# Kernel optimization log

Measured on AMD Instinct MI355X. Metric: run time of the kernel, lower is better.

## Reference

```python
import jax, jax.numpy as jnp
import numpy as np

N_NODES = 20000
N_INPUT = 64
K_MAX = 12
BITS = 64
N_OUT = 10
BATCH = 64
T = 128


def setup_inputs() -> dict:
    key = jax.random.key(0)
    ks = jax.random.split(key, 8)
    x = jax.random.randint(ks[0], (BATCH, T, BITS), 0, 2, dtype=jnp.int32)
    w_in = jax.random.randint(ks[1], (BITS, N_INPUT), 0, 2, dtype=jnp.int32)
    adj_list = jax.random.randint(ks[2], (N_NODES, K_MAX), 0, N_NODES, dtype=jnp.int32)
    adj_mask = jax.random.randint(ks[3], (N_NODES, K_MAX), 0, 2, dtype=jnp.int32)
    lut = jax.random.randint(ks[4], (N_NODES, 2 ** K_MAX), 0, 2, dtype=jnp.int32)
    init_states = jax.random.randint(ks[5], (1, N_NODES), 0, 2, dtype=jnp.int32)
    W_out = jax.random.normal(ks[6], (N_OUT, N_NODES - N_INPUT), dtype=jnp.float32) * 0.02
    b_out = jnp.zeros((N_OUT,), dtype=jnp.float32)
    return {"x": x, "w_in": w_in, "adj_list": adj_list, "adj_mask": adj_mask,
            "lut": lut, "init_states": init_states, "W_out": W_out, "b_out": b_out}


def reference(x, w_in, adj_list, adj_mask, lut, init_states, W_out, b_out):
    B, T_, bits = x.shape
    N, k = adj_list.shape
    I = w_in.shape[1]
    # powers_of_2, big-endian order as in make_minimal_powers_of_two (flip)
    powers = (2 ** jnp.arange(k - 1, -1, -1)).astype(jnp.int32)  # [k]
    no_neigh = ~(adj_mask.astype(bool).any(axis=1))              # [N] nodes w/o neighbours keep state
    node_ids = jnp.arange(N)
    states0 = jnp.broadcast_to(init_states, (B, N)).astype(jnp.int32)

    def step(states, x_t):
        # inject input: bipartite mapping of input bits onto first I nodes (OR-combine)
        u = ((x_t @ w_in) > 0).astype(jnp.int32)                 # [B, I]
        states = states.at[:, :I].set(u)
        # gather incoming neighbour states per node (irregular gather)
        neigh = jnp.take(states, adj_list, axis=1)               # [B, N, k]
        neigh = neigh * adj_mask[None, :, :]
        # bit-pack into LUT index
        idx = (neigh * powers[None, None, :]).sum(axis=-1)       # [B, N], < 2^k
        new = lut[node_ids[None, :], idx]                        # [B, N] LUT lookup
        new = jnp.where(no_neigh[None, :], states, new)
        return new, None

    states, _ = jax.lax.scan(step, states0, jnp.swapaxes(x, 0, 1))
    # readout on reservoir (non-input) nodes at final timestep
    feats = states[:, I:].astype(jnp.float32)                    # [B, N-I]
    out = jax.nn.sigmoid(feats @ W_out.T + b_out)                # [B, n_outputs]
    return out
```

## Files before the change

### kernel.cpp

```cpp
#include <hip/hip_runtime.h>
#include <cstdint>
#include <cstddef>


#define N_NODES   20000
#define N_INPUT   64
#define K_MAX     12
#define T_STEPS   128
#define N_BATCH   64
#define N_OUT     10
#define N_FEAT    (N_NODES - N_INPUT)
#define DUMMY_NODE 20000
#define ST_STRIDE 20008
#define R_DEPTH   (T_STEPS + 1)

#define NBLK 256
#define NTHR 1024
#define NPB  78
#define NPB_PAD 80
#define GO_CNT 8
#define AS     32

typedef unsigned long long u64;

#define A_LOAD(p)    __hip_atomic_load((p), __ATOMIC_RELAXED, __HIP_MEMORY_SCOPE_AGENT)
#define A_STORE(p,v) __hip_atomic_store((p), (v), __ATOMIC_RELAXED, __HIP_MEMORY_SCOPE_AGENT)

__global__ __launch_bounds__(256) void pack_x_kernel(const int* __restrict__ x,
                                                     u64* __restrict__ xp) {
  const int t = blockIdx.x;
  const int wave = threadIdx.x >> 6, lane = threadIdx.x & 63;
  for (int b = wave; b < N_BATCH; b += 4) {
    int v = x[((size_t)b * T_STEPS + t) * 64 + lane];
    u64 bal = __ballot(v != 0);
    if (lane == 0) xp[(size_t)t * N_BATCH + b] = bal;
  }
}

__global__ __launch_bounds__(256) void init_kernel(const int* __restrict__ inis,
                                                   const int* __restrict__ w_in,
                                                   u64* __restrict__ ring,
                                                   u64* __restrict__ wcol,
                                                   unsigned* __restrict__ arr,
                                                   unsigned* __restrict__ go) {
  if (blockIdx.x < 79) {
    int n = blockIdx.x * 256 + threadIdx.x;
    if (n >= N_INPUT && n < N_NODES)
      ring[n] = (inis[n] != 0) ? ~0ull : 0ull;
  } else {
    const int wave = threadIdx.x >> 6, lane = threadIdx.x & 63;
    for (int i = wave; i < 64; i += 4) {
      int wv = w_in[(size_t)lane * 64 + i];
      u64 wc = __ballot(wv != 0);
      if (lane == 0) wcol[i] = wc;
    }
    if (threadIdx.x < R_DEPTH)
      ring[(size_t)threadIdx.x * ST_STRIDE + DUMMY_NODE] = 0ull;
    arr[threadIdx.x * AS] = 0u;
    if (threadIdx.x < GO_CNT) go[threadIdx.x * AS] = 0u;
  }
}

__global__ __launch_bounds__(64) void u_pre_kernel(const u64* __restrict__ xp,
                                                   const u64* __restrict__ wcol,
                                                   u64* __restrict__ u_all) {
  const int t = blockIdx.x, lane = threadIdx.x;
  u64 xw = xp[(size_t)t * N_BATCH + lane];
  for (int i = 0; i < 64; i++) {
    u64 ub = __ballot((xw & wcol[i]) != 0);
    if (lane == 0) u_all[(size_t)t * 64 + i] = ub;
  }
}

__device__ __forceinline__ u64 bit_transpose64(u64 w, int lane) {
  const u64 LO0 = 0x00000000FFFFFFFFull, LO1 = 0x0000FFFF0000FFFFull,
            LO2 = 0x00FF00FF00FF00FFull, LO3 = 0x0F0F0F0F0F0F0F0Full,
            LO4 = 0x3333333333333333ull, LO5 = 0x5555555555555555ull;
#define XP_STAGE(d, LO)                                                  \
  {                                                                      \
    u64 p = (u64)__shfl_xor((long long)w, (d), 64);                      \
    if (lane & (d)) w = ((p >> (d)) & (LO)) | (w & ~(LO));               \
    else            w = (w & (LO)) | ((p << (d)) & ~(LO));               \
  }
  XP_STAGE(32, LO0) XP_STAGE(16, LO1) XP_STAGE(8, LO2)
  XP_STAGE(4,  LO3) XP_STAGE(2,  LO4) XP_STAGE(1, LO5)
#undef XP_STAGE
  return w;
}

__global__ __launch_bounds__(NTHR) void reservoir_kernel(
    const int* __restrict__ lut, const int* __restrict__ adj,
    const int* __restrict__ mask, const int* __restrict__ inis,
    const u64* __restrict__ u_all, u64* __restrict__ ring,
    unsigned* __restrict__ arr, unsigned* __restrict__ go) {
  __shared__ u64 lut_lds[NPB_PAD * 64];
  __shared__ int adj_lds[NPB_PAD * K_MAX];
  __shared__ unsigned char hn_lds[NPB_PAD];
  __shared__ volatile unsigned lds_scan[4];

  const int bi = blockIdx.x;
  const int tid = threadIdx.x;
  const int wave = tid >> 6, lane = tid & 63;
  const int base = N_INPUT + bi * NPB;
  const int nloc = min(NPB, N_NODES - base);

  if (wave == 0) __builtin_amdgcn_fence(__ATOMIC_ACQUIRE, "agent");

  if (tid < NPB_PAD) {
    int i = tid, h = 0;
    if (i < nloc) {
      for (int j = 0; j < K_MAX; j++) {
        int m = mask[(size_t)(base + i) * K_MAX + j];
        int a = adj[(size_t)(base + i) * K_MAX + j];
        adj_lds[i * K_MAX + (K_MAX - 1 - j)] = m ? a : DUMMY_NODE;
        h |= m;
      }
    } else {
      for (int j = 0; j < K_MAX; j++) adj_lds[i * K_MAX + j] = DUMMY_NODE;
    }
    hn_lds[i] = (unsigned char)(h ? 1 : 0);
  }
  if (tid < 4) lds_scan[tid] = 0u;

  const int nwords = nloc * 64;
  const int* lp = lut + (size_t)base * 4096;
  for (int w0 = wave * 8; w0 < nwords; w0 += 128) {
    int v[8];
#pragma unroll
    for (int q = 0; q < 8; q++) {
      int widx = w0 + q;
      v[q] = (widx < nwords) ? lp[(size_t)widx * 64 + lane] : 0;
    }
#pragma unroll
    for (int q = 0; q < 8; q++) {
      int widx = w0 + q;
      u64 bal = __ballot(v[q] != 0);
      if (lane == 0 && widx < nwords) lut_lds[widx] = bal;
    }
  }
  __syncthreads();

  const int l0 = wave * 5;
  const int cnt5 = min(5, nloc - l0);
  const int a_reg = (lane < 60) ? adj_lds[l0 * K_MAX + lane] : DUMMY_NODE;
  const bool store_ln = (lane < cnt5);
  const bool myhn = store_ln && hn_lds[l0 + lane];
  u64 mystate = 0;
  if (store_ln) mystate = (inis[base + l0 + lane] != 0) ? ~0ull : 0ull;

  for (int s = 0; s < T_STEPS; s++) {
    const u64* slot_cur = ring + (size_t)s * ST_STRIDE;
    u64* slot_nxt      = ring + (size_t)(s + 1) * ST_STRIDE;

    if (cnt5 > 0) {
      u64 w = 0;
      if (lane < 60) {
        const u64* p = (a_reg < N_INPUT) ? (u_all + (size_t)s * 64 + a_reg)
                                         : (slot_cur + a_reg);
        w = *p;
      }
      w = bit_transpose64(w, lane);

      u64 keep = 0;
#pragma unroll
      for (int i = 0; i < 5; i++) {
        if (i < cnt5) {
          unsigned idx = (unsigned)(w >> (12 * i)) & 0xFFFu;
          u64 g = lut_lds[(l0 + i) * 64 + (idx >> 6)];
          u64 res = __ballot((g >> (idx & 63)) & 1ull);
          if (lane == i) keep = res;
        }
      }
      if (store_ln) {
        u64 newS = myhn ? keep : mystate;
        mystate = newS;
        A_STORE(&slot_nxt[base + l0 + lane], newS);
      }
    }

    if (s != T_STEPS - 1) {
      const unsigned e = (unsigned)(s + 1);
      __syncthreads();
      if (wave == 0 && lane == 0) A_STORE(&arr[bi * AS], e);
      if (bi == 0 && wave < 4) {
        const int idx = (wave * 64 + lane) * AS;
        for (;;) {
          unsigned v = A_LOAD(&arr[idx]);
          if (__all(v >= e)) break;
        }
        if (lane == 0) lds_scan[wave] = e;
      }
      if (bi == 0 && wave == 0) {
        while (lds_scan[0] < e || lds_scan[1] < e ||
               lds_scan[2] < e || lds_scan[3] < e) {}
        if (lane < GO_CNT) A_STORE(&go[lane * AS], e);
      }
      if (wave == 0) {
        while (A_LOAD(&go[(bi & (GO_CNT - 1)) * AS]) < e) {}
      }
      __syncthreads();
    }
  }
}

__global__ __launch_bounds__(256) void readout_kernel(const u64* __restrict__ st,
                                                      const float* __restrict__ Wout,
                                                      const float* __restrict__ bout,
                                                      float* __restrict__ out) {
  const int b = blockIdx.x / N_OUT;
  const int o = blockIdx.x % N_OUT;
  float acc = 0.f;
  for (int n = threadIdx.x; n < N_FEAT; n += 256) {
    u64 s = st[N_INPUT + n];
    float w = Wout[(size_t)o * N_FEAT + n];
    acc += ((s >> b) & 1ull) ? w : 0.f;
  }
  for (int off = 32; off > 0; off >>= 1) acc += __shfl_down(acc, off);
  __shared__ float red[4];
  const int wave = threadIdx.x >> 6, lane = threadIdx.x & 63;
  if (lane == 0) red[wave] = acc;
  __syncthreads();
  if (threadIdx.x == 0) {
    float tot = red[0] + red[1] + red[2] + red[3] + bout[o];
    out[(size_t)b * N_OUT + o] = 1.f / (1.f + __expf(-tot));
  }
}

extern "C" void kernel_launch(void* const* d_in, const int* in_sizes, int n_in,
                              void* d_out, int out_size, void* d_ws, size_t ws_size,
                              hipStream_t stream) {
  const int* x    = (const int*)d_in[0];
  const int* w_in = (const int*)d_in[1];
  const int* adj  = (const int*)d_in[2];
  const int* mask = (const int*)d_in[3];
  const int* lut  = (const int*)d_in[4];
  const int* inis = (const int*)d_in[5];
  const float* Wout = (const float*)d_in[6];
  const float* bout = (const float*)d_in[7];
  float* out = (float*)d_out;

  char* ws = (char*)d_ws;
  size_t off = 0;
  auto alloc = [&](size_t bytes) -> void* {
    void* p = ws + off;
    off += (bytes + 255) & ~(size_t)255;
    return p;
  };
  u64* ring  = (u64*)alloc((size_t)R_DEPTH * ST_STRIDE * 8);
  u64* xp    = (u64*)alloc((size_t)T_STEPS * N_BATCH * 8);
  u64* wcol  = (u64*)alloc(64 * 8);
  u64* u_all = (u64*)alloc((size_t)T_STEPS * 64 * 8);
  unsigned* arr = (unsigned*)alloc((size_t)NBLK * AS * 4);
  unsigned* go  = (unsigned*)alloc((size_t)GO_CNT * AS * 4);
  (void)ws_size; (void)in_sizes; (void)n_in; (void)out_size;

  hipLaunchKernelGGL(pack_x_kernel, dim3(T_STEPS), dim3(256), 0, stream, x, xp);
  hipLaunchKernelGGL(init_kernel, dim3(80), dim3(256), 0, stream,
                     inis, w_in, ring, wcol, arr, go);
  hipLaunchKernelGGL(u_pre_kernel, dim3(T_STEPS), dim3(64), 0, stream,
                     xp, wcol, u_all);

  void* args[] = {(void*)&lut, (void*)&adj, (void*)&mask, (void*)&inis,
                  (void*)&u_all, (void*)&ring, (void*)&arr, (void*)&go};
  hipLaunchCooperativeKernel((const void*)reservoir_kernel,
                             dim3(NBLK), dim3(NTHR), args, 0, stream);

  hipLaunchKernelGGL(readout_kernel, dim3(N_BATCH * N_OUT), dim3(256), 0, stream,
                     ring + (size_t)T_STEPS * ST_STRIDE, Wout, bout, out);
}
```

Before: 1.052 ms.

## Replace two-level arrive/go grid barrier with distributed atomic counter barrier

Replaces the per-step grid barrier, where block 0 gathered 256 arrival flags and then broadcast go flags, with 64 packed counters that blocks atomically increment and that every block polls directly. This removes the serial gather-then-broadcast hop through block 0 on each of the 127 steps. In exchange all 256 blocks poll the same 64 words in one cache line, and the cross-block ordering of state stores now depends on workgroup-scope fences around relaxed atomics, which may be too weak for visibility across compute units.

```diff
diff --git a/kernel.cpp b/kernel.cpp
--- a/kernel.cpp
+++ b/kernel.cpp
@@ -18,13 +18,13 @@
 #define NTHR 1024
 #define NPB  78
 #define NPB_PAD 80
-#define GO_CNT 8
-#define AS     32
+#define BAR_N 64
 
 typedef unsigned long long u64;
 
 #define A_LOAD(p)    __hip_atomic_load((p), __ATOMIC_RELAXED, __HIP_MEMORY_SCOPE_AGENT)
 #define A_STORE(p,v) __hip_atomic_store((p), (v), __ATOMIC_RELAXED, __HIP_MEMORY_SCOPE_AGENT)
+#define A_RMW(p,v)   __hip_atomic_fetch_add((p), (v), __ATOMIC_RELAXED, __HIP_MEMORY_SCOPE_AGENT)
 
 __global__ __launch_bounds__(256) void pack_x_kernel(const int* __restrict__ x,
                                                      u64* __restrict__ xp) {
@@ -41,8 +41,7 @@
                                                    const int* __restrict__ w_in,
                                                    u64* __restrict__ ring,
                                                    u64* __restrict__ wcol,
-                                                   unsigned* __restrict__ arr,
-                                                   unsigned* __restrict__ go) {
+                                                   unsigned* __restrict__ arr) {
   if (blockIdx.x < 79) {
     int n = blockIdx.x * 256 + threadIdx.x;
     if (n >= N_INPUT && n < N_NODES)
@@ -56,8 +55,7 @@
     }
     if (threadIdx.x < R_DEPTH)
       ring[(size_t)threadIdx.x * ST_STRIDE + DUMMY_NODE] = 0ull;
-    arr[threadIdx.x * AS] = 0u;
-    if (threadIdx.x < GO_CNT) go[threadIdx.x * AS] = 0u;
+    if (threadIdx.x < BAR_N) arr[threadIdx.x] = 0u;
   }
 }
 
@@ -92,11 +90,10 @@
     const int* __restrict__ lut, const int* __restrict__ adj,
     const int* __restrict__ mask, const int* __restrict__ inis,
     const u64* __restrict__ u_all, u64* __restrict__ ring,
-    unsigned* __restrict__ arr, unsigned* __restrict__ go) {
+    unsigned* __restrict__ arr) {
   __shared__ u64 lut_lds[NPB_PAD * 64];
   __shared__ int adj_lds[NPB_PAD * K_MAX];
   __shared__ unsigned char hn_lds[NPB_PAD];
-  __shared__ volatile unsigned lds_scan[4];
 
   const int bi = blockIdx.x;
   const int tid = threadIdx.x;
@@ -120,7 +117,6 @@
     }
     hn_lds[i] = (unsigned char)(h ? 1 : 0);
   }
-  if (tid < 4) lds_scan[tid] = 0u;
 
   const int nwords = nloc * 64;
   const int* lp = lut + (size_t)base * 4096;
@@ -179,25 +175,18 @@
     }
 
     if (s != T_STEPS - 1) {
-      const unsigned e = (unsigned)(s + 1);
+      const unsigned tgt = (unsigned)(s + 1) * (NBLK / BAR_N);
       __syncthreads();
-      if (wave == 0 && lane == 0) A_STORE(&arr[bi * AS], e);
-      if (bi == 0 && wave < 4) {
-        const int idx = (wave * 64 + lane) * AS;
+      __builtin_amdgcn_fence(__ATOMIC_RELEASE, "workgroup");
+      if (tid == 0)
+        A_RMW(&arr[bi & (BAR_N - 1)], 1u);
+      if (wave == 0) {
         for (;;) {
-          unsigned v = A_LOAD(&arr[idx]);
-          if (__all(v >= e)) break;
+          unsigned v = A_LOAD(&arr[lane]);
+          if (__all(v >= tgt)) break;
         }
-        if (lane == 0) lds_scan[wave] = e;
-      }
-      if (bi == 0 && wave == 0) {
-        while (lds_scan[0] < e || lds_scan[1] < e ||
-               lds_scan[2] < e || lds_scan[3] < e) {}
-        if (lane < GO_CNT) A_STORE(&go[lane * AS], e);
-      }
-      if (wave == 0) {
-        while (A_LOAD(&go[(bi & (GO_CNT - 1)) * AS]) < e) {}
-      }
+      }
+      __builtin_amdgcn_fence(__ATOMIC_ACQUIRE, "workgroup");
       __syncthreads();
     }
   }
@@ -250,18 +239,17 @@
   u64* xp    = (u64*)alloc((size_t)T_STEPS * N_BATCH * 8);
   u64* wcol  = (u64*)alloc(64 * 8);
   u64* u_all = (u64*)alloc((size_t)T_STEPS * 64 * 8);
-  unsigned* arr = (unsigned*)alloc((size_t)NBLK * AS * 4);
-  unsigned* go  = (unsigned*)alloc((size_t)GO_CNT * AS * 4);
+  unsigned* arr = (unsigned*)alloc((size_t)BAR_N * 4);
   (void)ws_size; (void)in_sizes; (void)n_in; (void)out_size;
 
   hipLaunchKernelGGL(pack_x_kernel, dim3(T_STEPS), dim3(256), 0, stream, x, xp);
   hipLaunchKernelGGL(init_kernel, dim3(80), dim3(256), 0, stream,
-                     inis, w_in, ring, wcol, arr, go);
+                     inis, w_in, ring, wcol, arr);
   hipLaunchKernelGGL(u_pre_kernel, dim3(T_STEPS), dim3(64), 0, stream,
                      xp, wcol, u_all);
 
   void* args[] = {(void*)&lut, (void*)&adj, (void*)&mask, (void*)&inis,
-                  (void*)&u_all, (void*)&ring, (void*)&arr, (void*)&go};
+                  (void*)&u_all, (void*)&ring, (void*)&arr};
   hipLaunchCooperativeKernel((const void*)reservoir_kernel,
                              dim3(NBLK), dim3(NTHR), args, 0, stream);
 
```

Measured after the change: 1.752 ms. +66.5%, slower.
